# Performance work log

Hardware: AMD Instinct MI355X
Metric: run time of the kernel (lower is better)

Reference implementation:

```python
import jax, jax.numpy as jnp
import numpy as np

IN_CH = 256
BOT = IN_CH // 2  # bottleneck channels
B, W, H = 4, 64, 64


def setup_inputs() -> dict:
    key = jax.random.key(0)
    ks = jax.random.split(key, 10)
    s_in = 1.0 / np.sqrt(IN_CH)   # torch Conv2d default init scale (kaiming-ish bound)
    s_bt = 1.0 / np.sqrt(BOT)
    return {
        "X": jax.random.normal(ks[0], (B, IN_CH, W, H), dtype=jnp.float32),
        "Wq": jax.random.uniform(ks[1], (BOT, IN_CH), jnp.float32, -s_in, s_in),
        "bq": jax.random.uniform(ks[2], (BOT,), jnp.float32, -s_in, s_in),
        "Wk": jax.random.uniform(ks[3], (BOT, IN_CH), jnp.float32, -s_in, s_in),
        "bk": jax.random.uniform(ks[4], (BOT,), jnp.float32, -s_in, s_in),
        "Wv": jax.random.uniform(ks[5], (BOT, IN_CH), jnp.float32, -s_in, s_in),
        "bv": jax.random.uniform(ks[6], (BOT,), jnp.float32, -s_in, s_in),
        "Wo": jax.random.uniform(ks[7], (IN_CH, BOT), jnp.float32, -s_bt, s_bt),
        "bo": jax.random.uniform(ks[8], (IN_CH,), jnp.float32, -s_bt, s_bt),
        "gamma": 0.1 * jax.random.normal(ks[9], (1,), dtype=jnp.float32),
    }


def reference(X, Wq, bq, Wk, bk, Wv, bv, Wo, bo, gamma):
    b, c, w, h = X.shape
    n = w * h
    Xf = X.reshape(b, c, n)  # [b, c, n] — 1x1 conv == per-pixel linear
    q = jnp.einsum('oc,bcn->bon', Wq, Xf) + bq[None, :, None]  # [b, c/2, n]
    k = jnp.einsum('oc,bcn->bon', Wk, Xf) + bk[None, :, None]
    v = jnp.einsum('oc,bcn->bon', Wv, Xf) + bv[None, :, None]
    # score[b,i,j] = sum_c q[b,c,i] * k[b,c,j]; softmax over dim=1 (query index i)
    score = jnp.einsum('bci,bcj->bij', q, k)          # [b, n, n]
    attn = jax.nn.softmax(score, axis=1)
    out = jnp.einsum('bci,bij->bcj', v, attn)         # [b, c/2, n]
    out = jnp.einsum('oc,bcn->bon', Wo, out) + bo[None, :, None]  # [b, c, n]
    out = out.reshape(b, c, w, h)
    return gamma[0] * out + X
```

## Files before the change

### kernel.cpp

```cpp
#include <hip/hip_runtime.h>
#include <math.h>

#define NBATCH 4
#define CIN    256
#define CBOT   128
#define NPIX   4096
#define NPART  4
#define LOG2E  1.44269504f

typedef __attribute__((ext_vector_type(4))) float f32x4;
typedef __attribute__((ext_vector_type(8))) short bf16x8;

__device__ __forceinline__ unsigned short f2bf(float f) {
    union { float f; unsigned u; } v; v.f = f;
    unsigned r = (v.u + 0x7FFFu + ((v.u >> 16) & 1u)) >> 16;
    return (unsigned short)r;
}
__device__ __forceinline__ unsigned pk2bf(float a, float b) {
#if __has_builtin(__builtin_amdgcn_cvt_pk_bf16_f32)
    auto r = __builtin_amdgcn_cvt_pk_bf16_f32(a, b);
    unsigned u; __builtin_memcpy(&u, &r, 4); return u;
#else
    unsigned r;
    asm("v_cvt_pk_bf16_f32 %0, %1, %2" : "=v"(r) : "v"(a), "v"(b));
    return r;
#endif
}
__device__ __forceinline__ float fexp2(float x) {
#if __has_builtin(__builtin_amdgcn_exp2f)
    return __builtin_amdgcn_exp2f(x);
#else
    float r;
    asm("v_exp_f32 %0, %1" : "=v"(r) : "v"(x));
    return r;
#endif
}
__device__ __forceinline__ void plswap32(unsigned &a, unsigned &b) {
#if __has_builtin(__builtin_amdgcn_permlane32_swap)
    auto r = __builtin_amdgcn_permlane32_swap(a, b, false, false);
    a = (unsigned)r[0]; b = (unsigned)r[1];
#else
    asm volatile("v_permlane32_swap_b32 %0, %1" : "+v"(a), "+v"(b));
#endif
}
__device__ __forceinline__ void plswap16(unsigned &a, unsigned &b) {
#if __has_builtin(__builtin_amdgcn_permlane16_swap)
    auto r = __builtin_amdgcn_permlane16_swap(a, b, false, false);
    a = (unsigned)r[0]; b = (unsigned)r[1];
#else
    asm volatile("v_permlane16_swap_b32 %0, %1" : "+v"(a), "+v"(b));
#endif
}

__global__ __launch_bounds__(256) void k_wcvt(
    const float* __restrict__ Wq, const float* __restrict__ Wk,
    const float* __restrict__ Wv, const float* __restrict__ Wo,
    unsigned short* __restrict__ Wb)
{
    const int f4 = (blockIdx.x * 256 + threadIdx.x) * 4;
    const int reg = f4 >> 15, loc = f4 & 32767;
    const float* __restrict__ W = (reg == 0) ? Wq : (reg == 1) ? Wk : (reg == 2) ? Wv : Wo;
    const float sc = (reg == 1) ? LOG2E : 1.f;
    float4 v = *(const float4*)(W + loc);
    uint2 u;
    u.x = pk2bf(v.x * sc, v.y * sc);
    u.y = pk2bf(v.z * sc, v.w * sc);
    *(uint2*)&Wb[f4] = u;
}

__global__ __launch_bounds__(256) void k_qkvx(
    const float* __restrict__ X,
    const unsigned short* __restrict__ Wb,
    const float* __restrict__ bq, const float* __restrict__ bk,
    const float* __restrict__ bv,
    unsigned short* __restrict__ Qt, unsigned short* __restrict__ Kt,
    unsigned short* __restrict__ Vt)
{
    __shared__ __align__(16) unsigned short Xs[32][264];
    const int tid = threadIdx.x;
    const int wv = tid >> 6, lane = tid & 63;
    const int grp = lane & 15, quad = lane >> 4;
    const int pbase = blockIdx.x * 32;
    const int b     = blockIdx.y;
    const float* __restrict__ Xg = X + (size_t)b * CIN * NPIX + pbase;

#pragma unroll
    for (int k = 0; k < 8; ++k) {
        int f = tid + 256 * k;
        int c = f >> 3, pg = (f & 7) << 2;
        float4 v = *(const float4*)(Xg + (size_t)c * NPIX + pg);
        unsigned uxy = pk2bf(v.x, v.y);
        unsigned uzw = pk2bf(v.z, v.w);
        Xs[pg + 0][c] = (unsigned short)uxy;
        Xs[pg + 1][c] = (unsigned short)(uxy >> 16);
        Xs[pg + 2][c] = (unsigned short)uzw;
        Xs[pg + 3][c] = (unsigned short)(uzw >> 16);
    }
    __syncthreads();

    const unsigned short* __restrict__ Wqb = Wb;
    const unsigned short* __restrict__ Wkb = Wb + 32768;
    const unsigned short* __restrict__ Wvb = Wb + 65536;
    const int obase = 32 * wv;

    f32x4 aQ[2][2], aK[2][2], aV[2][2];
#pragma unroll
    for (int mt = 0; mt < 2; ++mt)
#pragma unroll
        for (int nt = 0; nt < 2; ++nt) {
            aQ[mt][nt] = (f32x4)0.f; aK[mt][nt] = (f32x4)0.f; aV[mt][nt] = (f32x4)0.f;
        }

    for (int ks = 0; ks < 8; ++ks) {
        bf16x8 bx[2];
#pragma unroll
        for (int nt = 0; nt < 2; ++nt)
            bx[nt] = *(const bf16x8*)&Xs[nt * 16 + grp][ks * 32 + quad * 8];
        bf16x8 wq_[2], wk_[2], wv_[2];
#pragma unroll
        for (int mt = 0; mt < 2; ++mt) {
            const size_t roff = (size_t)(obase + mt * 16 + grp) * CIN + ks * 32 + quad * 8;
            wq_[mt] = *(const bf16x8*)&Wqb[roff];
            wk_[mt] = *(const bf16x8*)&Wkb[roff];
            wv_[mt] = *(const bf16x8*)&Wvb[roff];
        }
#pragma unroll
        for (int mt = 0; mt < 2; ++mt)
#pragma unroll
            for (int nt = 0; nt < 2; ++nt) {
                aQ[mt][nt] = __builtin_amdgcn_mfma_f32_16x16x32_bf16(wq_[mt], bx[nt], aQ[mt][nt], 0, 0, 0);
                aK[mt][nt] = __builtin_amdgcn_mfma_f32_16x16x32_bf16(wk_[mt], bx[nt], aK[mt][nt], 0, 0, 0);
                aV[mt][nt] = __builtin_amdgcn_mfma_f32_16x16x32_bf16(bx[mt], wv_[nt], aV[mt][nt], 0, 0, 0);
            }
    }

    unsigned short* Qb_ = Qt + (size_t)b * NPIX * CBOT;
    unsigned short* Kb_ = Kt + (size_t)b * NPIX * CBOT;
#pragma unroll
    for (int mt = 0; mt < 2; ++mt) {
        int o0 = obase + mt * 16 + quad * 4;
        float b4q[4], b4k[4];
#pragma unroll
        for (int r = 0; r < 4; ++r) { b4q[r] = bq[o0 + r]; b4k[r] = bk[o0 + r] * LOG2E; }
#pragma unroll
        for (int nt = 0; nt < 2; ++nt) {
            int p = pbase + nt * 16 + grp;
            uint2 uq, uk;
            uq.x = pk2bf(aQ[mt][nt][0] + b4q[0], aQ[mt][nt][1] + b4q[1]);
            uq.y = pk2bf(aQ[mt][nt][2] + b4q[2], aQ[mt][nt][3] + b4q[3]);
            uk.x = pk2bf(aK[mt][nt][0] + b4k[0], aK[mt][nt][1] + b4k[1]);
            uk.y = pk2bf(aK[mt][nt][2] + b4k[2], aK[mt][nt][3] + b4k[3]);
            *(uint2*)&Qb_[(size_t)p * CBOT + o0] = uq;
            *(uint2*)&Kb_[(size_t)p * CBOT + o0] = uk;
        }
    }
    unsigned short* Vb_ = Vt + (size_t)b * CBOT * NPIX;
#pragma unroll
    for (int nt = 0; nt < 2; ++nt) {
        int o = obase + nt * 16 + grp;
        float bb = bv[o];
#pragma unroll
        for (int mt = 0; mt < 2; ++mt) {
            int p0 = pbase + mt * 16 + quad * 4;
            uint2 u;
            u.x = pk2bf(aV[mt][nt][0] + bb, aV[mt][nt][1] + bb);
            u.y = pk2bf(aV[mt][nt][2] + bb, aV[mt][nt][3] + bb);
            *(uint2*)&Vb_[(size_t)o * NPIX + p0] = u;
        }
    }
}

__global__ __launch_bounds__(256, 3) void k_flash(
    const unsigned short* __restrict__ Qt,
    const unsigned short* __restrict__ Kt,
    const unsigned short* __restrict__ Vt,
    unsigned short* __restrict__ Opart,
    float* __restrict__ Lpart)
{
    __shared__ __align__(16) unsigned short Qs[64][136];
    __shared__ __align__(16) unsigned short Vs[128][72];
    const int tid  = threadIdx.x;
    const int wv   = tid >> 6, lane = tid & 63;
    const int grp  = lane & 15, quad = lane >> 4;

    const int x     = blockIdx.x;
    const int pbRaw = blockIdx.y * NBATCH + blockIdx.z;
    const int jp    = (x >> 3) + 4 * (pbRaw >> 1);
    const int pbN   = (x & 7) * 2 + (pbRaw & 1);
    const int part  = pbN >> 2;
    const int b     = pbN & 3;
    const int jblk  = jp * 128;
    const int tbeg  = part * 16;
    const int tend  = tbeg + 16;
    const unsigned short* __restrict__ Qb = Qt + (size_t)b * NPIX * CBOT;
    const unsigned short* __restrict__ Kb = Kt + (size_t)b * NPIX * CBOT;
    const unsigned short* __restrict__ Vb = Vt + (size_t)b * CBOT * NPIX;

    bf16x8 bk[2][4];
#pragma unroll
    for (int nt = 0; nt < 2; ++nt)
#pragma unroll
        for (int ks = 0; ks < 4; ++ks)
            bk[nt][ks] = *(const bf16x8*)&Kb[
                (size_t)(jblk + wv * 32 + nt * 16 + grp) * CBOT + ks * 32 + quad * 8];

    bf16x8 aones;
#pragma unroll
    for (int t = 0; t < 8; ++t) aones[t] = (short)0x3F80;

    f32x4 o[8][2];
#pragma unroll
    for (int ct = 0; ct < 8; ++ct) { o[ct][0] = (f32x4)0.f; o[ct][1] = (f32x4)0.f; }
    f32x4 lacc[2] = {(f32x4)0.f, (f32x4)0.f};

    const int qrow = tid >> 4, qch = tid & 15;
    const int vrow = tid >> 3, vch = tid & 7;

    {
        bf16x8 tq[4], tv[4];
#pragma unroll
        for (int k = 0; k < 4; ++k) {
            tq[k] = *(const bf16x8*)&Qb[(size_t)(tbeg * 64 + qrow + 16 * k) * CBOT + qch * 8];
            tv[k] = *(const bf16x8*)&Vb[(size_t)(vrow + 32 * k) * NPIX + tbeg * 64 + vch * 8];
        }
#pragma unroll
        for (int k = 0; k < 4; ++k) {
            *(bf16x8*)&Qs[qrow + 16 * k][qch * 8] = tq[k];
            *(bf16x8*)&Vs[vrow + 32 * k][vch * 8] = tv[k];
        }
    }
    __syncthreads();

    for (int it = tbeg; it < tend; ++it) {
        f32x4 sf[4][2];
#pragma unroll
        for (int mt = 0; mt < 4; ++mt) { sf[mt][0] = (f32x4)0.f; sf[mt][1] = (f32x4)0.f; }
        __builtin_amdgcn_s_setprio(1);
#pragma unroll
        for (int mt = 0; mt < 4; ++mt)
#pragma unroll
            for (int ks = 0; ks < 4; ++ks) {
                bf16x8 aq_ = *(const bf16x8*)&Qs[mt * 16 + grp][ks * 32 + quad * 8];
                sf[mt][0] = __builtin_amdgcn_mfma_f32_16x16x32_bf16(aq_, bk[0][ks], sf[mt][0], 0, 0, 0);
                sf[mt][1] = __builtin_amdgcn_mfma_f32_16x16x32_bf16(aq_, bk[1][ks], sf[mt][1], 0, 0, 0);
            }
        __builtin_amdgcn_s_setprio(0);

        bf16x8 pf[2][2];
#pragma unroll
        for (int nt = 0; nt < 2; ++nt)
#pragma unroll
            for (int h = 0; h < 2; ++h) {
                unsigned u0a = pk2bf(fexp2(sf[2 * h][nt][0]),     fexp2(sf[2 * h][nt][1]));
                unsigned u1a = pk2bf(fexp2(sf[2 * h][nt][2]),     fexp2(sf[2 * h][nt][3]));
                unsigned u0b = pk2bf(fexp2(sf[2 * h + 1][nt][0]), fexp2(sf[2 * h + 1][nt][1]));
                unsigned u1b = pk2bf(fexp2(sf[2 * h + 1][nt][2]), fexp2(sf[2 * h + 1][nt][3]));
                plswap32(u0a, u0b); plswap16(u0a, u0b);
                plswap32(u1a, u1b); plswap16(u1a, u1b);
                union { unsigned uu[4]; bf16x8 v; } cvt;
                cvt.uu[0] = u0a; cvt.uu[1] = u1a; cvt.uu[2] = u0b; cvt.uu[3] = u1b;
                pf[nt][h] = cvt.v;
            }

        __builtin_amdgcn_s_setprio(1);
#pragma unroll
        for (int ct = 0; ct < 8; ++ct)
#pragma unroll
            for (int h = 0; h < 2; ++h) {
                bf16x8 av_ = *(const bf16x8*)&Vs[ct * 16 + grp][h * 32 + quad * 8];
                o[ct][0] = __builtin_amdgcn_mfma_f32_16x16x32_bf16(av_, pf[0][h], o[ct][0], 0, 0, 0);
                o[ct][1] = __builtin_amdgcn_mfma_f32_16x16x32_bf16(av_, pf[1][h], o[ct][1], 0, 0, 0);
            }
#pragma unroll
        for (int nt = 0; nt < 2; ++nt) {
            lacc[nt] = __builtin_amdgcn_mfma_f32_16x16x32_bf16(aones, pf[nt][0], lacc[nt], 0, 0, 0);
            lacc[nt] = __builtin_amdgcn_mfma_f32_16x16x32_bf16(aones, pf[nt][1], lacc[nt], 0, 0, 0);
        }
        __builtin_amdgcn_s_setprio(0);

        if (it + 1 < tend) {
            bf16x8 tq[4], tv[4];
            const size_t i1 = (size_t)(it + 1) * 64;
#pragma unroll
            for (int k = 0; k < 4; ++k) {
                tq[k] = *(const bf16x8*)&Qb[(i1 + qrow + 16 * k) * CBOT + qch * 8];
                tv[k] = *(const bf16x8*)&Vb[(size_t)(vrow + 32 * k) * NPIX + i1 + vch * 8];
            }
            __syncthreads();
#pragma unroll
            for (int k = 0; k < 4; ++k) {
                *(bf16x8*)&Qs[qrow + 16 * k][qch * 8] = tq[k];
                *(bf16x8*)&Vs[vrow + 32 * k][vch * 8] = tv[k];
            }
            __syncthreads();
        }
    }

    const int pbI = part * NBATCH + b;
    unsigned short* Ob = Opart + ((size_t)pbI * NPIX + jblk) * CBOT;
#pragma unroll
    for (int nt = 0; nt < 2; ++nt) {
        const size_t jrow = (size_t)(wv * 32 + nt * 16 + grp) * CBOT;
#pragma unroll
        for (int ct = 0; ct < 8; ++ct) {
            uint2 uo;
            uo.x = pk2bf(o[ct][nt][0], o[ct][nt][1]);
            uo.y = pk2bf(o[ct][nt][2], o[ct][nt][3]);
            *(uint2*)&Ob[jrow + ct * 16 + quad * 4] = uo;
        }
    }
    if (quad == 0) {
#pragma unroll
        for (int nt = 0; nt < 2; ++nt)
            Lpart[(size_t)pbI * NPIX + jblk + wv * 32 + nt * 16 + grp] =
                lacc[nt][0];
    }
}

__global__ __launch_bounds__(256) void k_oproj(
    const unsigned short* __restrict__ Opart, const float* __restrict__ Lpart,
    const unsigned short* __restrict__ Wob, const float* __restrict__ bo,
    const float* __restrict__ gamma, const float* __restrict__ X,
    float* __restrict__ Out)
{
    const int tid = threadIdx.x;
    const int wv = tid >> 6, lane = tid & 63;
    const int grp = lane & 15, quad = lane >> 4;
    const int pbase = blockIdx.x * 32;
    const int b     = blockIdx.y;
    const int obase = 64 * wv;

    f32x4 acc[2][4];
#pragma unroll
    for (int mt = 0; mt < 2; ++mt)
#pragma unroll
        for (int nt = 0; nt < 4; ++nt) acc[mt][nt] = (f32x4)0.f;

    for (int ks = 0; ks < 4; ++ks) {
        bf16x8 bw[4];
#pragma unroll
        for (int nt = 0; nt < 4; ++nt)
            bw[nt] = *(const bf16x8*)&Wob[(size_t)(obase + nt * 16 + grp) * CBOT + ks * 32 + quad * 8];
#pragma unroll
        for (int mt = 0; mt < 2; ++mt) {
            int p = pbase + mt * 16 + grp;
#pragma unroll
            for (int part = 0; part < NPART; ++part) {
                bf16x8 ao = *(const bf16x8*)&Opart[
                    ((size_t)(part * NBATCH + b) * NPIX + p) * CBOT + ks * 32 + quad * 8];
#pragma unroll
                for (int nt = 0; nt < 4; ++nt)
                    acc[mt][nt] = __builtin_amdgcn_mfma_f32_16x16x32_bf16(ao, bw[nt], acc[mt][nt], 0, 0, 0);
            }
        }
    }

    float linv[2][4];
#pragma unroll
    for (int mt = 0; mt < 2; ++mt)
#pragma unroll
        for (int r = 0; r < 4; ++r) {
            int p = pbase + mt * 16 + quad * 4 + r;
            float ls = 0.f;
#pragma unroll
            for (int part = 0; part < NPART; ++part)
                ls += Lpart[(size_t)(part * NBATCH + b) * NPIX + p];
            linv[mt][r] = 1.f / ls;
        }
    float gm = gamma[0];
#pragma unroll
    for (int nt = 0; nt < 4; ++nt) {
        int o = obase + nt * 16 + grp;
        float bb = bo[o];
#pragma unroll
        for (int mt = 0; mt < 2; ++mt) {
            int p0 = pbase + mt * 16 + quad * 4;
            size_t base = (size_t)b * CIN * NPIX + (size_t)o * NPIX + p0;
            float4 x4 = *(const float4*)(X + base);
            float4 r4;
            r4.x = gm * (acc[mt][nt][0] * linv[mt][0] + bb) + x4.x;
            r4.y = gm * (acc[mt][nt][1] * linv[mt][1] + bb) + x4.y;
            r4.z = gm * (acc[mt][nt][2] * linv[mt][2] + bb) + x4.z;
            r4.w = gm * (acc[mt][nt][3] * linv[mt][3] + bb) + x4.w;
            *(float4*)(Out + base) = r4;
        }
    }
}

extern "C" void kernel_launch(void* const* d_in, const int* in_sizes, int n_in,
                              void* d_out, int out_size, void* d_ws, size_t ws_size,
                              hipStream_t stream)
{
    (void)in_sizes; (void)n_in; (void)out_size; (void)ws_size;
    const float* X     = (const float*)d_in[0];
    const float* Wq    = (const float*)d_in[1];
    const float* bq    = (const float*)d_in[2];
    const float* Wk    = (const float*)d_in[3];
    const float* bk    = (const float*)d_in[4];
    const float* Wv    = (const float*)d_in[5];
    const float* bv    = (const float*)d_in[6];
    const float* Wo    = (const float*)d_in[7];
    const float* bo    = (const float*)d_in[8];
    const float* gamma = (const float*)d_in[9];
    float* out = (float*)d_out;

    const size_t BNC = (size_t)NBATCH * NPIX * CBOT;
    unsigned short* Qt    = (unsigned short*)d_ws;
    unsigned short* Kt    = Qt + BNC;
    unsigned short* Vt    = Kt + BNC;
    unsigned short* Opart = Vt + BNC;
    float*          Lpart = (float*)(Opart + (size_t)NPART * BNC);
    unsigned short* Wb    = (unsigned short*)(Lpart + (size_t)NPART * NBATCH * NPIX);

    k_wcvt <<<dim3(128),               256, 0, stream>>>(Wq, Wk, Wv, Wo, Wb);
    k_qkvx <<<dim3(128, NBATCH),       256, 0, stream>>>(X, Wb, bq, bk, bv, Qt, Kt, Vt);
    k_flash<<<dim3(32, NPART, NBATCH), 256, 0, stream>>>(Qt, Kt, Vt, Opart, Lpart);
    k_oproj<<<dim3(128, NBATCH),       256, 0, stream>>>(Opart, Lpart, Wb + 98304, bo, gamma, X, out);
}
```

Baseline: 157.0 us.

## Double-buffer Q/V tiles in LDS and prefetch the next tile during softmax

Switches the flash kernel to two LDS buffers in dynamic shared memory for the Q and V tiles. The global loads for the next tile are issued right after the QK MFMAs and written into the alternate buffer after the PV MFMAs, so one barrier per iteration is enough. The exp/pack and PV MFMAs are also interleaved per half to shorten live ranges. LDS use per block roughly doubles and launch bounds drop from 3 to 2 blocks per SIMD, which can lower occupancy.

```diff
diff --git a/kernel.cpp b/kernel.cpp
--- a/kernel.cpp
+++ b/kernel.cpp
@@ -170,15 +170,16 @@
     }
 }
 
-__global__ __launch_bounds__(256, 3) void k_flash(
+__global__ __launch_bounds__(256, 2) void k_flash(
     const unsigned short* __restrict__ Qt,
     const unsigned short* __restrict__ Kt,
     const unsigned short* __restrict__ Vt,
     unsigned short* __restrict__ Opart,
     float* __restrict__ Lpart)
 {
-    __shared__ __align__(16) unsigned short Qs[64][136];
-    __shared__ __align__(16) unsigned short Vs[128][72];
+    extern __shared__ __align__(16) unsigned short lds[];
+#define QS(bi, r, c) lds[(bi) * 8704 + (r) * 136 + (c)]
+#define VS(bi, r, c) lds[17408 + (bi) * 9216 + (r) * 72 + (c)]
     const int tid  = threadIdx.x;
     const int wv   = tid >> 6, lane = tid & 63;
     const int grp  = lane & 15, quad = lane >> 4;
@@ -225,13 +226,16 @@
         }
 #pragma unroll
         for (int k = 0; k < 4; ++k) {
-            *(bf16x8*)&Qs[qrow + 16 * k][qch * 8] = tq[k];
-            *(bf16x8*)&Vs[vrow + 32 * k][vch * 8] = tv[k];
+            *(bf16x8*)&QS(0, qrow + 16 * k, qch * 8) = tq[k];
+            *(bf16x8*)&VS(0, vrow + 32 * k, vch * 8) = tv[k];
         }
     }
     __syncthreads();
 
     for (int it = tbeg; it < tend; ++it) {
+        const int cur = (it - tbeg) & 1;
+        const bool more = (it + 1 < tend);
+
         f32x4 sf[4][2];
 #pragma unroll
         for (int mt = 0; mt < 4; ++mt) { sf[mt][0] = (f32x4)0.f; sf[mt][1] = (f32x4)0.f; }
@@ -240,17 +244,27 @@
         for (int mt = 0; mt < 4; ++mt)
 #pragma unroll
             for (int ks = 0; ks < 4; ++ks) {
-                bf16x8 aq_ = *(const bf16x8*)&Qs[mt * 16 + grp][ks * 32 + quad * 8];
+                bf16x8 aq_ = *(const bf16x8*)&QS(cur, mt * 16 + grp, ks * 32 + quad * 8);
                 sf[mt][0] = __builtin_amdgcn_mfma_f32_16x16x32_bf16(aq_, bk[0][ks], sf[mt][0], 0, 0, 0);
                 sf[mt][1] = __builtin_amdgcn_mfma_f32_16x16x32_bf16(aq_, bk[1][ks], sf[mt][1], 0, 0, 0);
             }
         __builtin_amdgcn_s_setprio(0);
 
-        bf16x8 pf[2][2];
-#pragma unroll
-        for (int nt = 0; nt < 2; ++nt)
-#pragma unroll
-            for (int h = 0; h < 2; ++h) {
+        bf16x8 tq[4], tv[4];
+        if (more) {
+            const size_t i1 = (size_t)(it + 1) * 64;
+#pragma unroll
+            for (int k = 0; k < 4; ++k) {
+                tq[k] = *(const bf16x8*)&Qb[(i1 + qrow + 16 * k) * CBOT + qch * 8];
+                tv[k] = *(const bf16x8*)&Vb[(size_t)(vrow + 32 * k) * NPIX + i1 + vch * 8];
+            }
+        }
+
+#pragma unroll
+        for (int h = 0; h < 2; ++h) {
+            bf16x8 pf[2];
+#pragma unroll
+            for (int nt = 0; nt < 2; ++nt) {
                 unsigned u0a = pk2bf(fexp2(sf[2 * h][nt][0]),     fexp2(sf[2 * h][nt][1]));
                 unsigned u1a = pk2bf(fexp2(sf[2 * h][nt][2]),     fexp2(sf[2 * h][nt][3]));
                 unsigned u0b = pk2bf(fexp2(sf[2 * h + 1][nt][0]), fexp2(sf[2 * h + 1][nt][1]));
@@ -259,38 +273,26 @@
                 plswap32(u1a, u1b); plswap16(u1a, u1b);
                 union { unsigned uu[4]; bf16x8 v; } cvt;
                 cvt.uu[0] = u0a; cvt.uu[1] = u1a; cvt.uu[2] = u0b; cvt.uu[3] = u1b;
-                pf[nt][h] = cvt.v;
-            }
-
-        __builtin_amdgcn_s_setprio(1);
-#pragma unroll
-        for (int ct = 0; ct < 8; ++ct)
-#pragma unroll
-            for (int h = 0; h < 2; ++h) {
-                bf16x8 av_ = *(const bf16x8*)&Vs[ct * 16 + grp][h * 32 + quad * 8];
-                o[ct][0] = __builtin_amdgcn_mfma_f32_16x16x32_bf16(av_, pf[0][h], o[ct][0], 0, 0, 0);
-                o[ct][1] = __builtin_amdgcn_mfma_f32_16x16x32_bf16(av_, pf[1][h], o[ct][1], 0, 0, 0);
-            }
-#pragma unroll
-        for (int nt = 0; nt < 2; ++nt) {
-            lacc[nt] = __builtin_amdgcn_mfma_f32_16x16x32_bf16(aones, pf[nt][0], lacc[nt], 0, 0, 0);
-            lacc[nt] = __builtin_amdgcn_mfma_f32_16x16x32_bf16(aones, pf[nt][1], lacc[nt], 0, 0, 0);
-        }
-        __builtin_amdgcn_s_setprio(0);
-
-        if (it + 1 < tend) {
-            bf16x8 tq[4], tv[4];
-            const size_t i1 = (size_t)(it + 1) * 64;
+                pf[nt] = cvt.v;
+            }
+            __builtin_amdgcn_s_setprio(1);
+#pragma unroll
+            for (int ct = 0; ct < 8; ++ct) {
+                bf16x8 av_ = *(const bf16x8*)&VS(cur, ct * 16 + grp, h * 32 + quad * 8);
+                o[ct][0] = __builtin_amdgcn_mfma_f32_16x16x32_bf16(av_, pf[0], o[ct][0], 0, 0, 0);
+                o[ct][1] = __builtin_amdgcn_mfma_f32_16x16x32_bf16(av_, pf[1], o[ct][1], 0, 0, 0);
+            }
+#pragma unroll
+            for (int nt = 0; nt < 2; ++nt)
+                lacc[nt] = __builtin_amdgcn_mfma_f32_16x16x32_bf16(aones, pf[nt], lacc[nt], 0, 0, 0);
+            __builtin_amdgcn_s_setprio(0);
+        }
+
+        if (more) {
 #pragma unroll
             for (int k = 0; k < 4; ++k) {
-                tq[k] = *(const bf16x8*)&Qb[(i1 + qrow + 16 * k) * CBOT + qch * 8];
-                tv[k] = *(const bf16x8*)&Vb[(size_t)(vrow + 32 * k) * NPIX + i1 + vch * 8];
-            }
-            __syncthreads();
-#pragma unroll
-            for (int k = 0; k < 4; ++k) {
-                *(bf16x8*)&Qs[qrow + 16 * k][qch * 8] = tq[k];
-                *(bf16x8*)&Vs[vrow + 32 * k][vch * 8] = tv[k];
+                *(bf16x8*)&QS(cur ^ 1, qrow + 16 * k, qch * 8) = tq[k];
+                *(bf16x8*)&VS(cur ^ 1, vrow + 32 * k, vch * 8) = tv[k];
             }
             __syncthreads();
         }
@@ -315,6 +317,8 @@
             Lpart[(size_t)pbI * NPIX + jblk + wv * 32 + nt * 16 + grp] =
                 lacc[nt][0];
     }
+#undef QS
+#undef VS
 }
 
 __global__ __launch_bounds__(256) void k_oproj(
@@ -412,8 +416,10 @@
     float*          Lpart = (float*)(Opart + (size_t)NPART * BNC);
     unsigned short* Wb    = (unsigned short*)(Lpart + (size_t)NPART * NBATCH * NPIX);
 
-    k_wcvt <<<dim3(128),               256, 0, stream>>>(Wq, Wk, Wv, Wo, Wb);
-    k_qkvx <<<dim3(128, NBATCH),       256, 0, stream>>>(X, Wb, bq, bk, bv, Qt, Kt, Vt);
-    k_flash<<<dim3(32, NPART, NBATCH), 256, 0, stream>>>(Qt, Kt, Vt, Opart, Lpart);
-    k_oproj<<<dim3(128, NBATCH),       256, 0, stream>>>(Opart, Lpart, Wb + 98304, bo, gamma, X, out);
-}
+    const int flash_lds = 2 * (64 * 136 + 128 * 72) * 2;
+
+    k_wcvt <<<dim3(128),               256, 0,         stream>>>(Wq, Wk, Wv, Wo, Wb);
+    k_qkvx <<<dim3(128, NBATCH),       256, 0,         stream>>>(X, Wb, bq, bk, bv, Qt, Kt, Vt);
+    k_flash<<<dim3(32, NPART, NBATCH), 256, flash_lds, stream>>>(Qt, Kt, Vt, Opart, Lpart);
+    k_oproj<<<dim3(128, NBATCH),       256, 0,         stream>>>(Opart, Lpart, Wb + 98304, bo, gamma, X, out);
+}
```

Result: no change. 158.2 us (+0.7%).
